# Performance work log

Hardware: AMD Instinct MI355X
Metric: run time of the kernel (lower is better)

The kernel has to match this reference:

```python
import jax, jax.numpy as jnp
import numpy as np

N = 50000       # nodes
E = 800000      # edges (avg degree 16)
D_IN = 128
D_H = 128
D_OUT = 64


def setup_inputs() -> dict:
    key = jax.random.key(0)
    ks = jax.random.split(key, 8)
    x = jax.random.normal(ks[0], (N, D_IN), dtype=jnp.float32)
    edge_index = jax.random.randint(ks[1], (2, E), 0, N)
    W1 = jax.random.normal(ks[2], (D_IN, D_H), dtype=jnp.float32) / np.sqrt(D_IN)
    b1 = jnp.zeros((D_H,), dtype=jnp.float32)
    W2 = jax.random.normal(ks[3], (D_H, D_H), dtype=jnp.float32) / np.sqrt(D_H)
    b2 = jnp.zeros((D_H,), dtype=jnp.float32)
    Wfc = jax.random.normal(ks[4], (D_H, D_OUT), dtype=jnp.float32) / np.sqrt(D_H)
    bfc = jnp.zeros((D_OUT,), dtype=jnp.float32)
    return {"x": x, "edge_index": edge_index, "W1": W1, "b1": b1,
            "W2": W2, "b2": b2, "Wfc": Wfc, "bfc": bfc}


def reference(x, edge_index, W1, b1, W2, b2, Wfc, bfc):
    n = x.shape[0]
    # GCNConv (PyG default): add self-loops, symmetric normalization
    loops = jnp.arange(n, dtype=edge_index.dtype)
    src = jnp.concatenate([edge_index[0], loops])
    dst = jnp.concatenate([edge_index[1], loops])
    deg = jax.ops.segment_sum(jnp.ones(src.shape, x.dtype), dst, num_segments=n)
    dinv = jnp.where(deg > 0, jax.lax.rsqrt(deg), jnp.zeros_like(deg))
    norm = dinv[src] * dinv[dst]  # [E + N]

    def gcn_conv(h, W, b):
        hw = h @ W                              # transform first (smaller gather)
        msg = hw[src] * norm[:, None]           # gather + scale
        return jax.ops.segment_sum(msg, dst, num_segments=n) + b  # scatter-add

    h = jax.nn.relu(gcn_conv(x, W1, b1))   # dropout_prob=0 -> identity
    h = jax.nn.relu(gcn_conv(h, W2, b2))
    pooled = jnp.max(h, axis=0)            # custom_global_max_pool over nodes
    return pooled @ Wfc + bfc              # [D_OUT]
```

## Files before the change

### kernel.cpp

```cpp
#include <hip/hip_runtime.h>
#include <cstdint>
#include <cstddef>

typedef unsigned int uint;
typedef unsigned short ushort;

__device__ __forceinline__ ushort f2bf(float f) {
    uint u = __float_as_uint(f);
    u = u + 0x7FFFu + ((u >> 16) & 1u);
    return (ushort)(u >> 16);
}
__device__ __forceinline__ float bf_lo(uint u) { return __uint_as_float((u & 0xFFFFu) << 16); }
__device__ __forceinline__ float bf_hi(uint u) { return __uint_as_float(u & 0xFFFF0000u); }


__global__ __launch_bounds__(256) void k_count(const int* __restrict__ dst,
                                               int* __restrict__ cnt,
                                               int* __restrict__ rank, int E) {
    int e4 = (blockIdx.x * 256 + threadIdx.x) * 4;
    if (e4 + 3 < E) {
        int4 d = *reinterpret_cast<const int4*>(&dst[e4]);
        int4 r;
        r.x = atomicAdd(&cnt[d.x], 1);
        r.y = atomicAdd(&cnt[d.y], 1);
        r.z = atomicAdd(&cnt[d.z], 1);
        r.w = atomicAdd(&cnt[d.w], 1);
        *reinterpret_cast<int4*>(&rank[e4]) = r;
    } else {
        for (int e = e4; e < E; e++)
            rank[e] = atomicAdd(&cnt[dst[e]], 1);
    }
}

__global__ __launch_bounds__(256) void k_block_reduce(const int* __restrict__ cnt,
                                                      int* __restrict__ bsum, int n) {
    __shared__ int sd[256];
    int i = blockIdx.x * 256 + threadIdx.x;
    sd[threadIdx.x] = (i < n) ? cnt[i] : 0;
    __syncthreads();
    for (int s = 128; s > 0; s >>= 1) {
        if (threadIdx.x < s) sd[threadIdx.x] += sd[threadIdx.x + s];
        __syncthreads();
    }
    if (threadIdx.x == 0) bsum[blockIdx.x] = sd[0];
}

__global__ __launch_bounds__(256) void k_scan_write(const int* __restrict__ cnt,
                                                    const int* __restrict__ bsum,
                                                    int* __restrict__ rowptr,
                                                    float* __restrict__ dinv,
                                                    int n, int nb) {
    __shared__ int sd[256];
    int t = threadIdx.x;
    sd[t] = (t < (int)blockIdx.x && t < nb) ? bsum[t] : 0;
    __syncthreads();
    for (int s = 128; s > 0; s >>= 1) {
        if (t < s) sd[t] += sd[t + s];
        __syncthreads();
    }
    int prefix = sd[0];
    __syncthreads();
    int i = blockIdx.x * 256 + t;
    int v = (i < n) ? cnt[i] : 0;
    sd[t] = v;
    __syncthreads();
    for (int off = 1; off < 256; off <<= 1) {
        int add = (t >= off) ? sd[t - off] : 0;
        __syncthreads();
        sd[t] += add;
        __syncthreads();
    }
    int excl = sd[t] - v + prefix;
    if (i < n) {
        rowptr[i] = excl;
        dinv[i] = rsqrtf((float)v + 1.0f);
    }
}

__global__ __launch_bounds__(256) void k_scatter(const int* __restrict__ src,
                                                 const int* __restrict__ dst,
                                                 const int* __restrict__ rowptr,
                                                 const int* __restrict__ rank,
                                                 const float* __restrict__ dinv,
                                                 int2* __restrict__ eSW, int E) {
    int e4 = (blockIdx.x * 256 + threadIdx.x) * 4;
    if (e4 + 3 < E) {
        int4 s = *reinterpret_cast<const int4*>(&src[e4]);
        int4 d = *reinterpret_cast<const int4*>(&dst[e4]);
        int4 r = *reinterpret_cast<const int4*>(&rank[e4]);
        int2 p0, p1, p2, p3;
        p0.x = s.x; p0.y = __float_as_int(dinv[s.x] * dinv[d.x]);
        p1.x = s.y; p1.y = __float_as_int(dinv[s.y] * dinv[d.y]);
        p2.x = s.z; p2.y = __float_as_int(dinv[s.z] * dinv[d.z]);
        p3.x = s.w; p3.y = __float_as_int(dinv[s.w] * dinv[d.w]);
        eSW[rowptr[d.x] + r.x] = p0;
        eSW[rowptr[d.y] + r.y] = p1;
        eSW[rowptr[d.z] + r.z] = p2;
        eSW[rowptr[d.w] + r.w] = p3;
    } else {
        for (int e = e4; e < E; e++) {
            int s = src[e], d = dst[e];
            int2 pp; pp.x = s; pp.y = __float_as_int(dinv[s] * dinv[d]);
            eSW[rowptr[d] + rank[e]] = pp;
        }
    }
}


#define AP 68

__global__ __launch_bounds__(256, 4) void k_gemm128(const float* __restrict__ A,
                                                    const float* __restrict__ Wg,
                                                    ushort* __restrict__ C, int nrows) {
    __shared__ float As[32 * AP];
    __shared__ float Ws[32 * 128];
    const int tid = threadIdx.x;
    const int tc = tid & 15;
    const int tr = tid >> 4;
    const int r0 = blockIdx.x * 64;

    float acc[4][8];
#pragma unroll
    for (int j = 0; j < 4; j++)
#pragma unroll
        for (int c = 0; c < 8; c++) acc[j][c] = 0.0f;

    const float4* A4 = reinterpret_cast<const float4*>(A);
    const float4* Wg4 = reinterpret_cast<const float4*>(Wg);
    float4* Ws4 = reinterpret_cast<float4*>(Ws);

    const int srow = tid >> 3;
    const int sk4 = tid & 7;

    for (int kc = 0; kc < 4; kc++) {
#pragma unroll
        for (int i = 0; i < 4; i++) Ws4[tid + 256 * i] = Wg4[kc * 1024 + tid + 256 * i];
#pragma unroll
        for (int pass = 0; pass < 2; pass++) {
            int rl = srow + pass * 32;
            int rg = r0 + rl;
            if (rg > nrows - 1) rg = nrows - 1;
            float4 av = A4[(size_t)rg * 32 + kc * 8 + sk4];
            int kb = sk4 * 4;
            As[(kb + 0) * AP + rl] = av.x;
            As[(kb + 1) * AP + rl] = av.y;
            As[(kb + 2) * AP + rl] = av.z;
            As[(kb + 3) * AP + rl] = av.w;
        }
        __syncthreads();

#pragma unroll 4
        for (int k = 0; k < 32; k++) {
            const float4 a = *reinterpret_cast<const float4*>(&As[k * AP + tr * 4]);
            const float4 w0 = *reinterpret_cast<const float4*>(&Ws[k * 128 + tc * 8]);
            const float4 w1 = *reinterpret_cast<const float4*>(&Ws[k * 128 + tc * 8 + 4]);
            const float av4[4] = {a.x, a.y, a.z, a.w};
            const float wv[8] = {w0.x, w0.y, w0.z, w0.w, w1.x, w1.y, w1.z, w1.w};
#pragma unroll
            for (int j = 0; j < 4; j++)
#pragma unroll
                for (int c = 0; c < 8; c++)
                    acc[j][c] = fmaf(av4[j], wv[c], acc[j][c]);
        }
        __syncthreads();
    }

#pragma unroll
    for (int j = 0; j < 4; j++) {
        const int r = r0 + tr * 4 + j;
        if (r < nrows) {
            uint4 o;
            o.x = (uint)f2bf(acc[j][0]) | ((uint)f2bf(acc[j][1]) << 16);
            o.y = (uint)f2bf(acc[j][2]) | ((uint)f2bf(acc[j][3]) << 16);
            o.z = (uint)f2bf(acc[j][4]) | ((uint)f2bf(acc[j][5]) << 16);
            o.w = (uint)f2bf(acc[j][6]) | ((uint)f2bf(acc[j][7]) << 16);
            *reinterpret_cast<uint4*>(&C[(size_t)r * 128 + tc * 8]) = o;
        }
    }
}


__global__ __launch_bounds__(256) void k_gather(const ushort* __restrict__ hw,
                                                const float* __restrict__ dinv,
                                                const int* __restrict__ rowptr,
                                                const int* __restrict__ cnt,
                                                const int2* __restrict__ eSW,
                                                const float* __restrict__ bias,
                                                float* __restrict__ outp, int n) {
    int wave = threadIdx.x >> 6;
    int lane = threadIdx.x & 63;
    int half = lane >> 5;
    int sub = lane & 31;
    int node = blockIdx.x * 4 + wave;
    if (node >= n) return;

    float di = dinv[node];
    int start = rowptr[node];
    int deg = cnt[node];

    const uint2* base2 = reinterpret_cast<const uint2*>(hw);
    float a0, a1, a2, a3;
    {
        uint2 u = base2[(size_t)node * 32 + sub];
        float sw = half ? 0.0f : di * di;
        a0 = bf_lo(u.x) * sw; a1 = bf_hi(u.x) * sw;
        a2 = bf_lo(u.y) * sw; a3 = bf_hi(u.y) * sw;
    }

    int j = 0;
    for (; j + 8 <= deg; j += 8) {
        int2 e[4]; uint2 u[4];
#pragma unroll
        for (int t = 0; t < 4; t++) e[t] = eSW[start + j + 2 * t + half];
#pragma unroll
        for (int t = 0; t < 4; t++) u[t] = base2[(size_t)e[t].x * 32 + sub];
#pragma unroll
        for (int t = 0; t < 4; t++) {
            float w = __int_as_float(e[t].y);
            a0 = fmaf(bf_lo(u[t].x), w, a0);
            a1 = fmaf(bf_hi(u[t].x), w, a1);
            a2 = fmaf(bf_lo(u[t].y), w, a2);
            a3 = fmaf(bf_hi(u[t].y), w, a3);
        }
    }
    for (; j < deg; j += 2) {
        int idx = j + half;
        bool ok = idx < deg;
        int2 e = eSW[start + (ok ? idx : deg - 1)];
        float w = ok ? __int_as_float(e.y) : 0.0f;
        uint2 u = base2[(size_t)e.x * 32 + sub];
        a0 = fmaf(bf_lo(u.x), w, a0);
        a1 = fmaf(bf_hi(u.x), w, a1);
        a2 = fmaf(bf_lo(u.y), w, a2);
        a3 = fmaf(bf_hi(u.y), w, a3);
    }

    a0 += __shfl_xor(a0, 32);
    a1 += __shfl_xor(a1, 32);
    a2 += __shfl_xor(a2, 32);
    a3 += __shfl_xor(a3, 32);

    if (half == 0) {
        float4 bb = reinterpret_cast<const float4*>(bias)[sub];
        float4 o;
        o.x = fmaxf(a0 + bb.x, 0.0f);
        o.y = fmaxf(a1 + bb.y, 0.0f);
        o.z = fmaxf(a2 + bb.z, 0.0f);
        o.w = fmaxf(a3 + bb.w, 0.0f);
        reinterpret_cast<float4*>(outp + (size_t)node * 128)[sub] = o;
    }
}


__global__ __launch_bounds__(256) void k_gather_pool(const ushort* __restrict__ hw,
                                                     const float* __restrict__ dinv,
                                                     const int* __restrict__ rowptr,
                                                     const int* __restrict__ cnt,
                                                     const int2* __restrict__ eSW,
                                                     const float* __restrict__ bias,
                                                     int* __restrict__ pooledPart, int n) {
    __shared__ int smax[128];
    int tid = threadIdx.x;
    int wave = tid >> 6;
    int lane = tid & 63;
    int half = lane >> 5;
    int sub = lane & 31;
    if (tid < 128) smax[tid] = 0;
    __syncthreads();

    int node = blockIdx.x * 4 + wave;
    if (node < n) {
        float di = dinv[node];
        int start = rowptr[node];
        int deg = cnt[node];

        const uint2* base2 = reinterpret_cast<const uint2*>(hw);
        float a0, a1, a2, a3;
        {
            uint2 u = base2[(size_t)node * 32 + sub];
            float sw = half ? 0.0f : di * di;
            a0 = bf_lo(u.x) * sw; a1 = bf_hi(u.x) * sw;
            a2 = bf_lo(u.y) * sw; a3 = bf_hi(u.y) * sw;
        }

        int j = 0;
        for (; j + 8 <= deg; j += 8) {
            int2 e[4]; uint2 u[4];
#pragma unroll
            for (int t = 0; t < 4; t++) e[t] = eSW[start + j + 2 * t + half];
#pragma unroll
            for (int t = 0; t < 4; t++) u[t] = base2[(size_t)e[t].x * 32 + sub];
#pragma unroll
            for (int t = 0; t < 4; t++) {
                float w = __int_as_float(e[t].y);
                a0 = fmaf(bf_lo(u[t].x), w, a0);
                a1 = fmaf(bf_hi(u[t].x), w, a1);
                a2 = fmaf(bf_lo(u[t].y), w, a2);
                a3 = fmaf(bf_hi(u[t].y), w, a3);
            }
        }
        for (; j < deg; j += 2) {
            int idx = j + half;
            bool ok = idx < deg;
            int2 e = eSW[start + (ok ? idx : deg - 1)];
            float w = ok ? __int_as_float(e.y) : 0.0f;
            uint2 u = base2[(size_t)e.x * 32 + sub];
            a0 = fmaf(bf_lo(u.x), w, a0);
            a1 = fmaf(bf_hi(u.x), w, a1);
            a2 = fmaf(bf_lo(u.y), w, a2);
            a3 = fmaf(bf_hi(u.y), w, a3);
        }

        a0 += __shfl_xor(a0, 32);
        a1 += __shfl_xor(a1, 32);
        a2 += __shfl_xor(a2, 32);
        a3 += __shfl_xor(a3, 32);

        if (half == 0) {
            float4 bb = reinterpret_cast<const float4*>(bias)[sub];
            a0 = fmaxf(a0 + bb.x, 0.0f);
            a1 = fmaxf(a1 + bb.y, 0.0f);
            a2 = fmaxf(a2 + bb.z, 0.0f);
            a3 = fmaxf(a3 + bb.w, 0.0f);
            atomicMax(&smax[sub * 4 + 0], __float_as_int(a0));
            atomicMax(&smax[sub * 4 + 1], __float_as_int(a1));
            atomicMax(&smax[sub * 4 + 2], __float_as_int(a2));
            atomicMax(&smax[sub * 4 + 3], __float_as_int(a3));
        }
    }
    __syncthreads();
    if (tid < 128) pooledPart[(size_t)blockIdx.x * 128 + tid] = smax[tid];
}


__global__ __launch_bounds__(256) void k_pool2(const int* __restrict__ pooledPart,
                                               int* __restrict__ pooledBits, int nPart) {
    __shared__ int smax[128];
    int tid = threadIdx.x;
    int c = tid & 127;
    int rh = tid >> 7;
    if (tid < 128) smax[tid] = 0;
    __syncthreads();
    int m = 0;
    for (int p = blockIdx.x * 2 + rh; p < nPart; p += gridDim.x * 2) {
        int v = pooledPart[(size_t)p * 128 + c];
        m = v > m ? v : m;
    }
    atomicMax(&smax[c], m);
    __syncthreads();
    if (tid < 128) atomicMax(&pooledBits[tid], smax[tid]);
}

__global__ __launch_bounds__(64) void k_fc(const int* __restrict__ pooledBits,
                                           const float* __restrict__ Wfc,
                                           const float* __restrict__ bfc,
                                           float* __restrict__ out) {
    int c = threadIdx.x;
    float acc = bfc[c];
    for (int k = 0; k < 128; k++)
        acc = fmaf(__int_as_float(pooledBits[k]), Wfc[k * 64 + c], acc);
    out[c] = acc;
}


extern "C" void kernel_launch(void* const* d_in, const int* in_sizes, int n_in,
                              void* d_out, int out_size, void* d_ws, size_t ws_size,
                              hipStream_t stream) {
    const float* x   = (const float*)d_in[0];
    const int* edges = (const int*)d_in[1];
    const float* W1  = (const float*)d_in[2];
    const float* b1  = (const float*)d_in[3];
    const float* W2  = (const float*)d_in[4];
    const float* b2  = (const float*)d_in[5];
    const float* Wfc = (const float*)d_in[6];
    const float* bfc = (const float*)d_in[7];
    float* out = (float*)d_out;

    const int N = in_sizes[0] / 128;
    const int E = in_sizes[1] / 2;
    const int* esrc_in = edges;
    const int* edst_in = edges + E;

    auto align256 = [](size_t v) { return (v + 255) & ~(size_t)255; };
    char* p = (char*)d_ws;
    size_t off = 0;
    int* cnt      = (int*)(p + off); off = align256(off + (size_t)N * 4);
    int* rowptr   = (int*)(p + off); off = align256(off + (size_t)N * 4);
    int* rank     = (int*)(p + off); off = align256(off + (size_t)E * 4);
    float* dinv   = (float*)(p + off); off = align256(off + (size_t)N * 4);
    int* bsum     = (int*)(p + off); off = align256(off + 256 * 4);
    int* pooled   = (int*)(p + off); off = align256(off + 128 * 4);
    int2* eSW     = (int2*)(p + off); off = align256(off + (size_t)E * 8);
    ushort* hwbuf = (ushort*)(p + off); off = align256(off + (size_t)N * 128 * 2);
    float* hbuf   = (float*)(p + off); off = align256(off + (size_t)N * 128 * 4);
    (void)ws_size; (void)n_in; (void)out_size;

    const int EB4 = (E / 4 + 255) / 256;
    const int NB = (N + 255) / 256;
    const int GB = (N + 63) / 64;
    const int HB = (N + 3) / 4;

    int* pooledPart = (int*)hbuf;

    hipMemsetAsync(cnt, 0, (size_t)N * 4, stream);

    k_count<<<EB4, 256, 0, stream>>>(edst_in, cnt, rank, E);
    k_block_reduce<<<NB, 256, 0, stream>>>(cnt, bsum, N);
    k_scan_write<<<NB, 256, 0, stream>>>(cnt, bsum, rowptr, dinv, N, NB);
    k_scatter<<<EB4, 256, 0, stream>>>(esrc_in, edst_in, rowptr, rank, dinv, eSW, E);

    k_gemm128<<<GB, 256, 0, stream>>>(x, W1, hwbuf, N);
    k_gather<<<HB, 256, 0, stream>>>(hwbuf, dinv, rowptr, cnt, eSW, b1, hbuf, N);
    k_gemm128<<<GB, 256, 0, stream>>>(hbuf, W2, hwbuf, N);
    k_gather_pool<<<HB, 256, 0, stream>>>(hwbuf, dinv, rowptr, cnt, eSW, b2, pooledPart, N);

    k_pool2<<<128, 256, 0, stream>>>(pooledPart, pooled, HB);
    k_fc<<<1, 64, 0, stream>>>(pooled, Wfc, bfc, out);
}
```

Before: 299.0 us.

## Store layer-1 activations in bf16, widen gather lanes, fuse scan and pool-FC

The intermediate hidden layer is now written as bf16 instead of fp32, and a new bf16-input GEMM reads it. This roughly halves activation traffic between the first gather and the second GEMM, at some cost in precision. The gather kernels now use 16 lanes per edge with 128-bit loads, so each wave processes four edges at once. The separate block-reduce kernel is dropped: each scan block recomputes its own prefix by summing all earlier counts, which costs redundant reads. Finally, the pool and FC kernels are merged using a last-block ticket, removing one launch.

New measurement: 324.6 us. 8.5% more time.

```diff
diff --git a/kernel.cpp b/kernel.cpp
--- a/kernel.cpp
+++ b/kernel.cpp
@@ -32,27 +32,15 @@
     }
 }
 
-__global__ __launch_bounds__(256) void k_block_reduce(const int* __restrict__ cnt,
-                                                      int* __restrict__ bsum, int n) {
-    __shared__ int sd[256];
-    int i = blockIdx.x * 256 + threadIdx.x;
-    sd[threadIdx.x] = (i < n) ? cnt[i] : 0;
-    __syncthreads();
-    for (int s = 128; s > 0; s >>= 1) {
-        if (threadIdx.x < s) sd[threadIdx.x] += sd[threadIdx.x + s];
-        __syncthreads();
-    }
-    if (threadIdx.x == 0) bsum[blockIdx.x] = sd[0];
-}
-
 __global__ __launch_bounds__(256) void k_scan_write(const int* __restrict__ cnt,
-                                                    const int* __restrict__ bsum,
                                                     int* __restrict__ rowptr,
-                                                    float* __restrict__ dinv,
-                                                    int n, int nb) {
+                                                    float* __restrict__ dinv, int n) {
     __shared__ int sd[256];
     int t = threadIdx.x;
-    sd[t] = (t < (int)blockIdx.x && t < nb) ? bsum[t] : 0;
+    int base = blockIdx.x * 256;
+    int acc = 0;
+    for (int i = t; i < base; i += 256) acc += cnt[i];
+    sd[t] = acc;
     __syncthreads();
     for (int s = 128; s > 0; s >>= 1) {
         if (t < s) sd[t] += sd[t + s];
@@ -60,7 +48,7 @@
     }
     int prefix = sd[0];
     __syncthreads();
-    int i = blockIdx.x * 256 + t;
+    int i = base + t;
     int v = (i < n) ? cnt[i] : 0;
     sd[t] = v;
     __syncthreads();
@@ -109,9 +97,9 @@
 
 #define AP 68
 
-__global__ __launch_bounds__(256, 4) void k_gemm128(const float* __restrict__ A,
-                                                    const float* __restrict__ Wg,
-                                                    ushort* __restrict__ C, int nrows) {
+__global__ __launch_bounds__(256, 4) void k_gemm128_f32(const float* __restrict__ A,
+                                                        const float* __restrict__ Wg,
+                                                        ushort* __restrict__ C, int nrows) {
     __shared__ float As[32 * AP];
     __shared__ float Ws[32 * 128];
     const int tid = threadIdx.x;
@@ -179,6 +167,78 @@
     }
 }
 
+__global__ __launch_bounds__(256, 4) void k_gemm128_bf16(const ushort* __restrict__ A,
+                                                         const float* __restrict__ Wg,
+                                                         ushort* __restrict__ C, int nrows) {
+    __shared__ float As[32 * AP];
+    __shared__ float Ws[32 * 128];
+    const int tid = threadIdx.x;
+    const int tc = tid & 15;
+    const int tr = tid >> 4;
+    const int r0 = blockIdx.x * 64;
+
+    float acc[4][8];
+#pragma unroll
+    for (int j = 0; j < 4; j++)
+#pragma unroll
+        for (int c = 0; c < 8; c++) acc[j][c] = 0.0f;
+
+    const uint4* A4 = reinterpret_cast<const uint4*>(A);
+    const float4* Wg4 = reinterpret_cast<const float4*>(Wg);
+    float4* Ws4 = reinterpret_cast<float4*>(Ws);
+
+    const int srow = tid >> 2;
+    const int sk = tid & 3;
+
+    for (int kc = 0; kc < 4; kc++) {
+#pragma unroll
+        for (int i = 0; i < 4; i++) Ws4[tid + 256 * i] = Wg4[kc * 1024 + tid + 256 * i];
+        {
+            int rg = r0 + srow;
+            if (rg > nrows - 1) rg = nrows - 1;
+            uint4 u = A4[(size_t)rg * 16 + kc * 4 + sk];
+            int kb = sk * 8;
+            As[(kb + 0) * AP + srow] = bf_lo(u.x);
+            As[(kb + 1) * AP + srow] = bf_hi(u.x);
+            As[(kb + 2) * AP + srow] = bf_lo(u.y);
+            As[(kb + 3) * AP + srow] = bf_hi(u.y);
+            As[(kb + 4) * AP + srow] = bf_lo(u.z);
+            As[(kb + 5) * AP + srow] = bf_hi(u.z);
+            As[(kb + 6) * AP + srow] = bf_lo(u.w);
+            As[(kb + 7) * AP + srow] = bf_hi(u.w);
+        }
+        __syncthreads();
+
+#pragma unroll 4
+        for (int k = 0; k < 32; k++) {
+            const float4 a = *reinterpret_cast<const float4*>(&As[k * AP + tr * 4]);
+            const float4 w0 = *reinterpret_cast<const float4*>(&Ws[k * 128 + tc * 8]);
+            const float4 w1 = *reinterpret_cast<const float4*>(&Ws[k * 128 + tc * 8 + 4]);
+            const float av4[4] = {a.x, a.y, a.z, a.w};
+            const float wv[8] = {w0.x, w0.y, w0.z, w0.w, w1.x, w1.y, w1.z, w1.w};
+#pragma unroll
+            for (int j = 0; j < 4; j++)
+#pragma unroll
+                for (int c = 0; c < 8; c++)
+                    acc[j][c] = fmaf(av4[j], wv[c], acc[j][c]);
+        }
+        __syncthreads();
+    }
+
+#pragma unroll
+    for (int j = 0; j < 4; j++) {
+        const int r = r0 + tr * 4 + j;
+        if (r < nrows) {
+            uint4 o;
+            o.x = (uint)f2bf(acc[j][0]) | ((uint)f2bf(acc[j][1]) << 16);
+            o.y = (uint)f2bf(acc[j][2]) | ((uint)f2bf(acc[j][3]) << 16);
+            o.z = (uint)f2bf(acc[j][4]) | ((uint)f2bf(acc[j][5]) << 16);
+            o.w = (uint)f2bf(acc[j][6]) | ((uint)f2bf(acc[j][7]) << 16);
+            *reinterpret_cast<uint4*>(&C[(size_t)r * 128 + tc * 8]) = o;
+        }
+    }
+}
+
 
 __global__ __launch_bounds__(256) void k_gather(const ushort* __restrict__ hw,
                                                 const float* __restrict__ dinv,
@@ -186,11 +246,11 @@
                                                 const int* __restrict__ cnt,
                                                 const int2* __restrict__ eSW,
                                                 const float* __restrict__ bias,
-                                                float* __restrict__ outp, int n) {
+                                                ushort* __restrict__ outp, int n) {
     int wave = threadIdx.x >> 6;
     int lane = threadIdx.x & 63;
-    int half = lane >> 5;
-    int sub = lane & 31;
+    int q = lane >> 4;
+    int sub = lane & 15;
     int node = blockIdx.x * 4 + wave;
     if (node >= n) return;
 
@@ -198,56 +258,65 @@
     int start = rowptr[node];
     int deg = cnt[node];
 
-    const uint2* base2 = reinterpret_cast<const uint2*>(hw);
-    float a0, a1, a2, a3;
+    const uint4* base4 = reinterpret_cast<const uint4*>(hw);
+    float a[8];
     {
-        uint2 u = base2[(size_t)node * 32 + sub];
-        float sw = half ? 0.0f : di * di;
-        a0 = bf_lo(u.x) * sw; a1 = bf_hi(u.x) * sw;
-        a2 = bf_lo(u.y) * sw; a3 = bf_hi(u.y) * sw;
+        uint4 u = base4[(size_t)node * 16 + sub];
+        float sw = (q == 0) ? di * di : 0.0f;
+        a[0] = bf_lo(u.x) * sw; a[1] = bf_hi(u.x) * sw;
+        a[2] = bf_lo(u.y) * sw; a[3] = bf_hi(u.y) * sw;
+        a[4] = bf_lo(u.z) * sw; a[5] = bf_hi(u.z) * sw;
+        a[6] = bf_lo(u.w) * sw; a[7] = bf_hi(u.w) * sw;
     }
 
     int j = 0;
     for (; j + 8 <= deg; j += 8) {
-        int2 e[4]; uint2 u[4];
-#pragma unroll
-        for (int t = 0; t < 4; t++) e[t] = eSW[start + j + 2 * t + half];
-#pragma unroll
-        for (int t = 0; t < 4; t++) u[t] = base2[(size_t)e[t].x * 32 + sub];
-#pragma unroll
-        for (int t = 0; t < 4; t++) {
-            float w = __int_as_float(e[t].y);
-            a0 = fmaf(bf_lo(u[t].x), w, a0);
-            a1 = fmaf(bf_hi(u[t].x), w, a1);
-            a2 = fmaf(bf_lo(u[t].y), w, a2);
-            a3 = fmaf(bf_hi(u[t].y), w, a3);
-        }
-    }
-    for (; j < deg; j += 2) {
-        int idx = j + half;
+        int2 e0 = eSW[start + j + q];
+        int2 e1 = eSW[start + j + 4 + q];
+        uint4 u0 = base4[(size_t)e0.x * 16 + sub];
+        uint4 u1 = base4[(size_t)e1.x * 16 + sub];
+        float w0 = __int_as_float(e0.y);
+        float w1 = __int_as_float(e1.y);
+        a[0] = fmaf(bf_lo(u0.x), w0, a[0]); a[1] = fmaf(bf_hi(u0.x), w0, a[1]);
+        a[2] = fmaf(bf_lo(u0.y), w0, a[2]); a[3] = fmaf(bf_hi(u0.y), w0, a[3]);
+        a[4] = fmaf(bf_lo(u0.z), w0, a[4]); a[5] = fmaf(bf_hi(u0.z), w0, a[5]);
+        a[6] = fmaf(bf_lo(u0.w), w0, a[6]); a[7] = fmaf(bf_hi(u0.w), w0, a[7]);
+        a[0] = fmaf(bf_lo(u1.x), w1, a[0]); a[1] = fmaf(bf_hi(u1.x), w1, a[1]);
+        a[2] = fmaf(bf_lo(u1.y), w1, a[2]); a[3] = fmaf(bf_hi(u1.y), w1, a[3]);
+        a[4] = fmaf(bf_lo(u1.z), w1, a[4]); a[5] = fmaf(bf_hi(u1.z), w1, a[5]);
+        a[6] = fmaf(bf_lo(u1.w), w1, a[6]); a[7] = fmaf(bf_hi(u1.w), w1, a[7]);
+    }
+    for (; j < deg; j += 4) {
+        int idx = j + q;
         bool ok = idx < deg;
         int2 e = eSW[start + (ok ? idx : deg - 1)];
         float w = ok ? __int_as_float(e.y) : 0.0f;
-        uint2 u = base2[(size_t)e.x * 32 + sub];
-        a0 = fmaf(bf_lo(u.x), w, a0);
-        a1 = fmaf(bf_hi(u.x), w, a1);
-        a2 = fmaf(bf_lo(u.y), w, a2);
-        a3 = fmaf(bf_hi(u.y), w, a3);
-    }
-
-    a0 += __shfl_xor(a0, 32);
-    a1 += __shfl_xor(a1, 32);
-    a2 += __shfl_xor(a2, 32);
-    a3 += __shfl_xor(a3, 32);
-
-    if (half == 0) {
-        float4 bb = reinterpret_cast<const float4*>(bias)[sub];
-        float4 o;
-        o.x = fmaxf(a0 + bb.x, 0.0f);
-        o.y = fmaxf(a1 + bb.y, 0.0f);
-        o.z = fmaxf(a2 + bb.z, 0.0f);
-        o.w = fmaxf(a3 + bb.w, 0.0f);
-        reinterpret_cast<float4*>(outp + (size_t)node * 128)[sub] = o;
+        uint4 u = base4[(size_t)e.x * 16 + sub];
+        a[0] = fmaf(bf_lo(u.x), w, a[0]); a[1] = fmaf(bf_hi(u.x), w, a[1]);
+        a[2] = fmaf(bf_lo(u.y), w, a[2]); a[3] = fmaf(bf_hi(u.y), w, a[3]);
+        a[4] = fmaf(bf_lo(u.z), w, a[4]); a[5] = fmaf(bf_hi(u.z), w, a[5]);
+        a[6] = fmaf(bf_lo(u.w), w, a[6]); a[7] = fmaf(bf_hi(u.w), w, a[7]);
+    }
+
+#pragma unroll
+    for (int k = 0; k < 8; k++) {
+        a[k] += __shfl_xor(a[k], 16);
+        a[k] += __shfl_xor(a[k], 32);
+    }
+
+    if (q == 0) {
+        float4 b0 = reinterpret_cast<const float4*>(bias)[sub * 2];
+        float4 b1 = reinterpret_cast<const float4*>(bias)[sub * 2 + 1];
+        float r0 = fmaxf(a[0] + b0.x, 0.0f), r1 = fmaxf(a[1] + b0.y, 0.0f);
+        float r2 = fmaxf(a[2] + b0.z, 0.0f), r3 = fmaxf(a[3] + b0.w, 0.0f);
+        float r4 = fmaxf(a[4] + b1.x, 0.0f), r5 = fmaxf(a[5] + b1.y, 0.0f);
+        float r6 = fmaxf(a[6] + b1.z, 0.0f), r7 = fmaxf(a[7] + b1.w, 0.0f);
+        uint4 o;
+        o.x = (uint)f2bf(r0) | ((uint)f2bf(r1) << 16);
+        o.y = (uint)f2bf(r2) | ((uint)f2bf(r3) << 16);
+        o.z = (uint)f2bf(r4) | ((uint)f2bf(r5) << 16);
+        o.w = (uint)f2bf(r6) | ((uint)f2bf(r7) << 16);
+        reinterpret_cast<uint4*>(outp)[(size_t)node * 16 + sub] = o;
     }
 }
 
@@ -263,8 +332,8 @@
     int tid = threadIdx.x;
     int wave = tid >> 6;
     int lane = tid & 63;
-    int half = lane >> 5;
-    int sub = lane & 31;
+    int q = lane >> 4;
+    int sub = lane & 15;
     if (tid < 128) smax[tid] = 0;
     __syncthreads();
 
@@ -274,58 +343,63 @@
         int start = rowptr[node];
         int deg = cnt[node];
 
-        const uint2* base2 = reinterpret_cast<const uint2*>(hw);
-        float a0, a1, a2, a3;
+        const uint4* base4 = reinterpret_cast<const uint4*>(hw);
+        float a[8];
         {
-            uint2 u = base2[(size_t)node * 32 + sub];
-            float sw = half ? 0.0f : di * di;
-            a0 = bf_lo(u.x) * sw; a1 = bf_hi(u.x) * sw;
-            a2 = bf_lo(u.y) * sw; a3 = bf_hi(u.y) * sw;
+            uint4 u = base4[(size_t)node * 16 + sub];
+            float sw = (q == 0) ? di * di : 0.0f;
+            a[0] = bf_lo(u.x) * sw; a[1] = bf_hi(u.x) * sw;
+            a[2] = bf_lo(u.y) * sw; a[3] = bf_hi(u.y) * sw;
+            a[4] = bf_lo(u.z) * sw; a[5] = bf_hi(u.z) * sw;
+            a[6] = bf_lo(u.w) * sw; a[7] = bf_hi(u.w) * sw;
         }
 
         int j = 0;
         for (; j + 8 <= deg; j += 8) {
-            int2 e[4]; uint2 u[4];
-#pragma unroll
-            for (int t = 0; t < 4; t++) e[t] = eSW[start + j + 2 * t + half];
-#pragma unroll
-            for (int t = 0; t < 4; t++) u[t] = base2[(size_t)e[t].x * 32 + sub];
-#pragma unroll
-            for (int t = 0; t < 4; t++) {
-                float w = __int_as_float(e[t].y);
-                a0 = fmaf(bf_lo(u[t].x), w, a0);
-                a1 = fmaf(bf_hi(u[t].x), w, a1);
-                a2 = fmaf(bf_lo(u[t].y), w, a2);
-                a3 = fmaf(bf_hi(u[t].y), w, a3);
-            }
-        }
-        for (; j < deg; j += 2) {
-            int idx = j + half;
+            int2 e0 = eSW[start + j + q];
+            int2 e1 = eSW[start + j + 4 + q];
+            uint4 u0 = base4[(size_t)e0.x * 16 + sub];
+            uint4 u1 = base4[(size_t)e1.x * 16 + sub];
+            float w0 = __int_as_float(e0.y);
+            float w1 = __int_as_float(e1.y);
+            a[0] = fmaf(bf_lo(u0.x), w0, a[0]); a[1] = fmaf(bf_hi(u0.x), w0, a[1]);
+            a[2] = fmaf(bf_lo(u0.y), w0, a[2]); a[3] = fmaf(bf_hi(u0.y), w0, a[3]);
+            a[4] = fmaf(bf_lo(u0.z), w0, a[4]); a[5] = fmaf(bf_hi(u0.z), w0, a[5]);
+            a[6] = fmaf(bf_lo(u0.w), w0, a[6]); a[7] = fmaf(bf_hi(u0.w), w0, a[7]);
+            a[0] = fmaf(bf_lo(u1.x), w1, a[0]); a[1] = fmaf(bf_hi(u1.x), w1, a[1]);
+            a[2] = fmaf(bf_lo(u1.y), w1, a[2]); a[3] = fmaf(bf_hi(u1.y), w1, a[3]);
+            a[4] = fmaf(bf_lo(u1.z), w1, a[4]); a[5] = fmaf(bf_hi(u1.z), w1, a[5]);
+            a[6] = fmaf(bf_lo(u1.w), w1, a[6]); a[7] = fmaf(bf_hi(u1.w), w1, a[7]);
+        }
+        for (; j < deg; j += 4) {
+            int idx = j + q;
             bool ok = idx < deg;
             int2 e = eSW[start + (ok ? idx : deg - 1)];
             float w = ok ? __int_as_float(e.y) : 0.0f;
-            uint2 u = base2[(size_t)e.x * 32 + sub];
-            a0 = fmaf(bf_lo(u.x), w, a0);
-            a1 = fmaf(bf_hi(u.x), w, a1);
-            a2 = fmaf(bf_lo(u.y), w, a2);
-            a3 = fmaf(bf_hi(u.y), w, a3);
-        }
-
-        a0 += __shfl_xor(a0, 32);
-        a1 += __shfl_xor(a1, 32);
-        a2 += __shfl_xor(a2, 32);
-        a3 += __shfl_xor(a3, 32);
-
-        if (half == 0) {
-            float4 bb = reinterpret_cast<const float4*>(bias)[sub];
-            a0 = fmaxf(a0 + bb.x, 0.0f);
-            a1 = fmaxf(a1 + bb.y, 0.0f);
-            a2 = fmaxf(a2 + bb.z, 0.0f);
-            a3 = fmaxf(a3 + bb.w, 0.0f);
-            atomicMax(&smax[sub * 4 + 0], __float_as_int(a0));
-            atomicMax(&smax[sub * 4 + 1], __float_as_int(a1));
-            atomicMax(&smax[sub * 4 + 2], __float_as_int(a2));
-            atomicMax(&smax[sub * 4 + 3], __float_as_int(a3));
+            uint4 u = base4[(size_t)e.x * 16 + sub];
+            a[0] = fmaf(bf_lo(u.x), w, a[0]); a[1] = fmaf(bf_hi(u.x), w, a[1]);
+            a[2] = fmaf(bf_lo(u.y), w, a[2]); a[3] = fmaf(bf_hi(u.y), w, a[3]);
+            a[4] = fmaf(bf_lo(u.z), w, a[4]); a[5] = fmaf(bf_hi(u.z), w, a[5]);
+            a[6] = fmaf(bf_lo(u.w), w, a[6]); a[7] = fmaf(bf_hi(u.w), w, a[7]);
+        }
+
+#pragma unroll
+        for (int k = 0; k < 8; k++) {
+            a[k] += __shfl_xor(a[k], 16);
+            a[k] += __shfl_xor(a[k], 32);
+        }
+
+        if (q == 0) {
+            float4 b0 = reinterpret_cast<const float4*>(bias)[sub * 2];
+            float4 b1 = reinterpret_cast<const float4*>(bias)[sub * 2 + 1];
+            float r[8];
+            r[0] = fmaxf(a[0] + b0.x, 0.0f); r[1] = fmaxf(a[1] + b0.y, 0.0f);
+            r[2] = fmaxf(a[2] + b0.z, 0.0f); r[3] = fmaxf(a[3] + b0.w, 0.0f);
+            r[4] = fmaxf(a[4] + b1.x, 0.0f); r[5] = fmaxf(a[5] + b1.y, 0.0f);
+            r[6] = fmaxf(a[6] + b1.z, 0.0f); r[7] = fmaxf(a[7] + b1.w, 0.0f);
+#pragma unroll
+            for (int k = 0; k < 8; k++)
+                atomicMax(&smax[sub * 8 + k], __float_as_int(r[k]));
         }
     }
     __syncthreads();
@@ -333,9 +407,14 @@
 }
 
 
-__global__ __launch_bounds__(256) void k_pool2(const int* __restrict__ pooledPart,
-                                               int* __restrict__ pooledBits, int nPart) {
+__global__ __launch_bounds__(256) void k_pool2fc(const int* __restrict__ pooledPart,
+                                                 int* __restrict__ pooledBits,
+                                                 int* __restrict__ ticket,
+                                                 const float* __restrict__ Wfc,
+                                                 const float* __restrict__ bfc,
+                                                 float* __restrict__ out, int nPart) {
     __shared__ int smax[128];
+    __shared__ int isLast;
     int tid = threadIdx.x;
     int c = tid & 127;
     int rh = tid >> 7;
@@ -349,17 +428,20 @@
     atomicMax(&smax[c], m);
     __syncthreads();
     if (tid < 128) atomicMax(&pooledBits[tid], smax[tid]);
-}
-
-__global__ __launch_bounds__(64) void k_fc(const int* __restrict__ pooledBits,
-                                           const float* __restrict__ Wfc,
-                                           const float* __restrict__ bfc,
-                                           float* __restrict__ out) {
-    int c = threadIdx.x;
-    float acc = bfc[c];
-    for (int k = 0; k < 128; k++)
-        acc = fmaf(__int_as_float(pooledBits[k]), Wfc[k * 64 + c], acc);
-    out[c] = acc;
+    __threadfence();
+    if (tid == 0) isLast = (atomicAdd(ticket, 1) == (int)gridDim.x - 1) ? 1 : 0;
+    __syncthreads();
+    if (isLast) {
+        __threadfence();
+        if (tid < 128) smax[tid] = atomicMax(&pooledBits[tid], 0);
+        __syncthreads();
+        if (tid < 64) {
+            float acc = bfc[tid];
+            for (int k = 0; k < 128; k++)
+                acc = fmaf(__int_as_float(smax[k]), Wfc[k * 64 + tid], acc);
+            out[tid] = acc;
+        }
+    }
 }
 
 
@@ -384,15 +466,15 @@
     auto align256 = [](size_t v) { return (v + 255) & ~(size_t)255; };
     char* p = (char*)d_ws;
     size_t off = 0;
-    int* cnt      = (int*)(p + off); off = align256(off + (size_t)N * 4);
+    int* cnt      = (int*)(p + off); off += (size_t)N * 4;
+    int* ticket   = (int*)(p + off); off = align256(off + 4);
     int* rowptr   = (int*)(p + off); off = align256(off + (size_t)N * 4);
     int* rank     = (int*)(p + off); off = align256(off + (size_t)E * 4);
     float* dinv   = (float*)(p + off); off = align256(off + (size_t)N * 4);
-    int* bsum     = (int*)(p + off); off = align256(off + 256 * 4);
     int* pooled   = (int*)(p + off); off = align256(off + 128 * 4);
     int2* eSW     = (int2*)(p + off); off = align256(off + (size_t)E * 8);
     ushort* hwbuf = (ushort*)(p + off); off = align256(off + (size_t)N * 128 * 2);
-    float* hbuf   = (float*)(p + off); off = align256(off + (size_t)N * 128 * 4);
+    ushort* h1buf = (ushort*)(p + off); off = align256(off + (size_t)N * 128 * 2);
     (void)ws_size; (void)n_in; (void)out_size;
 
     const int EB4 = (E / 4 + 255) / 256;
@@ -400,20 +482,18 @@
     const int GB = (N + 63) / 64;
     const int HB = (N + 3) / 4;
 
-    int* pooledPart = (int*)hbuf;
-
-    hipMemsetAsync(cnt, 0, (size_t)N * 4, stream);
+    int* pooledPart = (int*)h1buf;
+
+    hipMemsetAsync(cnt, 0, (size_t)N * 4 + 4, stream);
 
     k_count<<<EB4, 256, 0, stream>>>(edst_in, cnt, rank, E);
-    k_block_reduce<<<NB, 256, 0, stream>>>(cnt, bsum, N);
-    k_scan_write<<<NB, 256, 0, stream>>>(cnt, bsum, rowptr, dinv, N, NB);
+    k_scan_write<<<NB, 256, 0, stream>>>(cnt, rowptr, dinv, N);
     k_scatter<<<EB4, 256, 0, stream>>>(esrc_in, edst_in, rowptr, rank, dinv, eSW, E);
 
-    k_gemm128<<<GB, 256, 0, stream>>>(x, W1, hwbuf, N);
-    k_gather<<<HB, 256, 0, stream>>>(hwbuf, dinv, rowptr, cnt, eSW, b1, hbuf, N);
-    k_gemm128<<<GB, 256, 0, stream>>>(hbuf, W2, hwbuf, N);
+    k_gemm128_f32<<<GB, 256, 0, stream>>>(x, W1, hwbuf, N);
+    k_gather<<<HB, 256, 0, stream>>>(hwbuf, dinv, rowptr, cnt, eSW, b1, h1buf, N);
+    k_gemm128_bf16<<<GB, 256, 0, stream>>>(h1buf, W2, hwbuf, N);
     k_gather_pool<<<HB, 256, 0, stream>>>(hwbuf, dinv, rowptr, cnt, eSW, b2, pooledPart, N);
 
-    k_pool2<<<128, 256, 0, stream>>>(pooledPart, pooled, HB);
-    k_fc<<<1, 64, 0, stream>>>(pooled, Wfc, bfc, out);
-}
+    k_pool2fc<<<128, 256, 0, stream>>>(pooledPart, pooled, ticket, Wfc, bfc, out, HB);
+}
```
